# Performance work log

Hardware: AMD Instinct MI355X
Metric: run time of the kernel (lower is better)

The kernel has to match this reference:

```python
import jax, jax.numpy as jnp
import numpy as np

PI = 3.1415  # the module hard-codes 3.1415, not math.pi


def setup_inputs() -> dict:
    nt, ns, nh, ng = 1000, 1024, 64, 32
    key = jax.random.key(0)
    kP, kE, kT1, kT2, kxc, kW, kb = jax.random.split(key, 7)
    # physically plausible forcings: P, E >= 0; T2 > T1 always
    P = jax.random.uniform(kP, (nt, ns)) * 10.0
    E = jax.random.uniform(kE, (nt, ns)) * 5.0
    T1 = jax.random.normal(kT1, (nt, ns)) * 10.0
    T2 = T1 + jax.random.uniform(kT2, (nt, ns)) * 10.0 + 0.1
    x = jnp.stack([P, E, T1, T2], axis=-1)  # [nt, ns, 4]
    xc = jax.random.normal(kxc, (ns, ng))
    std = 1.0 / np.sqrt(nh)  # reset_parameters: uniform(-std, std)
    W3 = jax.random.uniform(kW, (nh * 4, ng), minval=-std, maxval=std)
    b3 = jax.random.uniform(kb, (nh * 4,), minval=-std, maxval=std)
    return {"x": x, "xc": xc, "W3": W3, "b3": b3}


def reference(x, xc, W3, b3):
    nh = W3.shape[0] // 4
    P, E, T1, T2 = x[..., 0], x[..., 1], x[..., 2], x[..., 3]  # each [nt, ns]
    Ta = (T1 + T2) * 0.5
    melted = T1 >= 0.0
    frozen = T2 <= 0.0
    masked = melted | frozen
    # NaN-safe arccos: out-of-range args occur exactly where masked overrides apply
    arg = jnp.where(masked, 0.0, jnp.clip((T1 + T2) / (T2 - T1), -1.0, 1.0))
    rP = 1.0 - jnp.arccos(arg) / PI
    rP = jnp.where(melted, 1.0, jnp.where(frozen, 0.0, rP))
    Ps = (1.0 - rP) * P  # snow fraction
    Pl = rP * P          # liquid fraction
    # static gates (fc3 on catchment attributes); dropout is identity in eval
    w = xc @ W3.T + b3  # [ns, 4*nh]
    gm = jnp.exp(w[:, :nh]) + 1.0
    ge = jax.nn.sigmoid(w[:, nh:2 * nh])
    go = jax.nn.sigmoid(w[:, 2 * nh:3 * nh])
    ga = jax.nn.softmax(w[:, 3 * nh:], axis=1)

    ns = P.shape[1]
    S0 = jnp.zeros((ns, nh), dtype=x.dtype)
    H0 = jnp.zeros((ns, nh), dtype=x.dtype)

    def step(carry, inp):
        S0, H0 = carry
        Ps_k, Pl_k, E_k, Ta_k = inp  # each [ns]
        Sm = jnp.minimum(S0, jax.nn.relu(Ta_k[:, None] * gm))  # snowmelt
        S = S0 + Ps_k[:, None]
        H = jax.nn.relu(H0 + Sm + Pl_k[:, None] - E_k[:, None] * ge)
        Q = H * go
        Y = jnp.sum(Q * ga, axis=1)  # [ns]
        return (S - Sm, H - Q), Y

    _, Yout = jax.lax.scan(step, (S0, H0), (Ps, Pl, E, Ta))
    return Yout  # [nt, ns]
```

## Files before the change

kernel.cpp:

```cpp
#include <hip/hip_runtime.h>
#include <math.h>

#define NH 64
#define NG 32
#define YROW 68

__global__ __launch_bounds__(128) void waternet_kernel(
    const float* __restrict__ x,
    const float* __restrict__ xc,
    const float* __restrict__ W3,
    const float* __restrict__ b3,
    float* __restrict__ out,
    int nt, int ns)
{
    const int b    = blockIdx.x;
    const int s    = (b & 7) * (ns >> 3) + (b >> 3);
    const int tid  = threadIdx.x;
    const int lane = tid & 63;
    const bool crit = (tid < 64);

    __shared__ float ytile[2][NH * YROW];
    __shared__ float scal[2][NH * 4];
    __shared__ float gqbuf[NH];

    float wq[4];
    #pragma unroll
    for (int q = 0; q < 4; ++q) {
        const float4* row = reinterpret_cast<const float4*>(W3 + (size_t)(q * NH + lane) * NG);
        const float4* xr  = reinterpret_cast<const float4*>(xc + (size_t)s * NG);
        float a = 0.f;
        #pragma unroll
        for (int g = 0; g < NG / 4; ++g) {
            const float4 w  = row[g];
            const float4 xv = xr[g];
            a = fmaf(w.x, xv.x, a); a = fmaf(w.y, xv.y, a);
            a = fmaf(w.z, xv.z, a); a = fmaf(w.w, xv.w, a);
        }
        wq[q] = a + b3[q * NH + lane];
    }
    const float gm = expf(wq[0]) + 1.0f;
    const float ge = 1.0f / (1.0f + expf(-wq[1]));
    const float go = 1.0f / (1.0f + expf(-wq[2]));
    float mx = wq[3];
    #pragma unroll
    for (int o = 32; o; o >>= 1) mx = fmaxf(mx, __shfl_xor(mx, o, 64));
    const float ex = expf(wq[3] - mx);
    float smx = ex;
    #pragma unroll
    for (int o = 32; o; o >>= 1) smx += __shfl_xor(smx, o, 64);
    const float ga = ex / smx;
    const float gq = go * ga;
    const float gk = 1.0f - go;

    if (!crit) gqbuf[lane] = gq;

    const int nchunk = (nt + NH - 1) / NH;

    #define PHASE_A(f, dst) { \
        const float P = (f).x, E = (f).y, T1 = (f).z, T2 = (f).w; \
        const float Ta  = 0.5f * (T1 + T2); \
        const float arg = fminf(1.f, fmaxf(-1.f, (T1 + T2) / (T2 - T1))); \
        const float aa  = fabsf(arg); \
        float p = fmaf(aa, -0.0012624911f, 0.0066700901f); \
        p = fmaf(aa, p, -0.0170881256f); p = fmaf(aa, p, 0.0308918810f); \
        p = fmaf(aa, p, -0.0501743046f); p = fmaf(aa, p, 0.0889789874f); \
        p = fmaf(aa, p, -0.2145988016f); p = fmaf(aa, p, 1.5707963050f); \
        const float rr0 = sqrtf(1.f - aa) * p; \
        const float ac  = (arg >= 0.f) ? rr0 : (3.14159265358979f - rr0); \
        const float rr  = 1.f - ac * (1.0f / 3.1415f);           \
        const float rP  = (T1 >= 0.f) ? 1.f : ((T2 <= 0.f) ? 0.f : rr); \
        float4 st; st.x = fmaxf(Ta, 0.f); st.y = (1.f - rP) * P; \
        st.z = rP * P;  st.w = E; \
        *reinterpret_cast<float4*>(&(dst)[lane * 4]) = st; \
    }

    #define LOAD8(dst, sp, j0) { \
        _Pragma("unroll") \
        for (int k = 0; k < 8; ++k) \
            dst[k] = *reinterpret_cast<const float4*>(&(sp)[((j0) + k) * 4]); \
    }

    #define STEP(sc) { \
        const float M  = (sc).x * gm; \
        const float Sm = fminf(S, M); \
        S = (S - Sm) + (sc).y; \
        const float t2 = Sm + (sc).z; \
        const float t3 = fmaf(-(sc).w, ge, t2); \
        Hc = fmaxf(fmaf(gk, Hc, t3), 0.f); \
    }

    if (!crit) {
        const int tp = min(lane, nt - 1);
        const float4 f = *reinterpret_cast<const float4*>(x + ((size_t)tp * ns + s) * 4);
        PHASE_A(f, scal[0])
    }
    __syncthreads();

    float S = 0.f, Hc = 0.f;

    #pragma unroll 1
    for (int c = 0; c < nchunk; ++c) {
        const int cnt = min(NH, nt - c * NH);
        if (crit) {
            const float* sp = scal[c & 1];
            float*       yb = &ytile[c & 1][lane * YROW];
            if (cnt == NH) {
                float4 sc[8], scn[8];
                LOAD8(sc, sp, 0)
                #pragma unroll
                for (int bb = 0; bb < 8; ++bb) {
                    if (bb < 7) LOAD8(scn, sp, (bb + 1) * 8)
                    float yv[8];
                    #pragma unroll
                    for (int k = 0; k < 8; ++k) { STEP(sc[k]) yv[k] = Hc; }
                    *reinterpret_cast<float4*>(yb + bb * 8)     = make_float4(yv[0], yv[1], yv[2], yv[3]);
                    *reinterpret_cast<float4*>(yb + bb * 8 + 4) = make_float4(yv[4], yv[5], yv[6], yv[7]);
                    if (bb < 7) {
                        #pragma unroll
                        for (int k = 0; k < 8; ++k) sc[k] = scn[k];
                    }
                }
            } else {
                const int nb = cnt / 8;
                for (int bb = 0; bb < nb; ++bb) {
                    float4 sc[8];
                    LOAD8(sc, sp, bb * 8)
                    float yv[8];
                    #pragma unroll
                    for (int k = 0; k < 8; ++k) { STEP(sc[k]) yv[k] = Hc; }
                    *reinterpret_cast<float4*>(yb + bb * 8)     = make_float4(yv[0], yv[1], yv[2], yv[3]);
                    *reinterpret_cast<float4*>(yb + bb * 8 + 4) = make_float4(yv[4], yv[5], yv[6], yv[7]);
                }
                for (int j = nb * 8; j < cnt; ++j) {
                    const float4 sc = *reinterpret_cast<const float4*>(&sp[j * 4]);
                    STEP(sc)
                    yb[j] = Hc;
                }
            }
        } else {
            const int tp = min((c + 1) * NH + lane, nt - 1);
            const float4 f = *reinterpret_cast<const float4*>(x + ((size_t)tp * ns + s) * 4);
            if (c >= 1) {
                const float* yr = ytile[(c - 1) & 1];
                float z0 = 0.f, z1 = 0.f, z2 = 0.f, z3 = 0.f;
                #pragma unroll
                for (int h = 0; h < NH; h += 4) {
                    z0 = fmaf(gqbuf[h + 0], yr[(h + 0) * YROW + lane], z0);
                    z1 = fmaf(gqbuf[h + 1], yr[(h + 1) * YROW + lane], z1);
                    z2 = fmaf(gqbuf[h + 2], yr[(h + 2) * YROW + lane], z2);
                    z3 = fmaf(gqbuf[h + 3], yr[(h + 3) * YROW + lane], z3);
                }
                out[(size_t)((c - 1) * NH + lane) * ns + s] = (z0 + z1) + (z2 + z3);
            }
            PHASE_A(f, scal[(c + 1) & 1])
        }
        __syncthreads();
    }

    if (!crit) {
        const int c   = nchunk - 1;
        const int cnt = nt - c * NH;
        const float* yr = ytile[c & 1];
        float z0 = 0.f, z1 = 0.f, z2 = 0.f, z3 = 0.f;
        #pragma unroll
        for (int h = 0; h < NH; h += 4) {
            z0 = fmaf(gqbuf[h + 0], yr[(h + 0) * YROW + lane], z0);
            z1 = fmaf(gqbuf[h + 1], yr[(h + 1) * YROW + lane], z1);
            z2 = fmaf(gqbuf[h + 2], yr[(h + 2) * YROW + lane], z2);
            z3 = fmaf(gqbuf[h + 3], yr[(h + 3) * YROW + lane], z3);
        }
        if (lane < cnt)
            out[(size_t)(c * NH + lane) * ns + s] = (z0 + z1) + (z2 + z3);
    }
    #undef PHASE_A
    #undef LOAD8
    #undef STEP
}

extern "C" void kernel_launch(void* const* d_in, const int* in_sizes, int n_in,
                              void* d_out, int out_size, void* d_ws, size_t ws_size,
                              hipStream_t stream) {
    const float* x  = (const float*)d_in[0];
    const float* xc = (const float*)d_in[1];
    const float* W3 = (const float*)d_in[2];
    const float* b3 = (const float*)d_in[3];
    float* out = (float*)d_out;

    const int nh = in_sizes[3] / 4;
    const int ng = in_sizes[2] / (4 * nh);
    const int ns = in_sizes[1] / ng;
    const int nt = in_sizes[0] / (ns * 4);

    waternet_kernel<<<dim3(ns), dim3(128), 0, stream>>>(x, xc, W3, b3, out, nt, ns);
}
```

Before: 101.7 us.

## Move forcing preprocessing into critical wave and broadcast via readlane

The critical wavefront now loads and preprocesses its own chunk of forcings in registers, then broadcasts per-timestep values to all lanes with readlane instead of reading float4 records from shared memory. The reduction wave likewise broadcasts the gq weights with readlane instead of reading an LDS buffer. This removes the scal/gqbuf shared arrays and the LDS loads from the serial recurrence. In exchange the critical wave takes on the arccos preprocessing and global load latency, which were previously overlapped on the helper wave, and readlane into SGPRs may serialize differently.

```diff
diff --git a/kernel.cpp b/kernel.cpp
--- a/kernel.cpp
+++ b/kernel.cpp
@@ -4,6 +4,10 @@
 #define NH 64
 #define NG 32
 #define YROW 68
+
+__device__ __forceinline__ float bcast(float v, int l) {
+    return __int_as_float(__builtin_amdgcn_readlane(__float_as_int(v), l));
+}
 
 __global__ __launch_bounds__(128) void waternet_kernel(
     const float* __restrict__ x,
@@ -20,8 +24,6 @@
     const bool crit = (tid < 64);
 
     __shared__ float ytile[2][NH * YROW];
-    __shared__ float scal[2][NH * 4];
-    __shared__ float gqbuf[NH];
 
     float wq[4];
     #pragma unroll
@@ -52,12 +54,11 @@
     const float gq = go * ga;
     const float gk = 1.0f - go;
 
-    if (!crit) gqbuf[lane] = gq;
-
     const int nchunk = (nt + NH - 1) / NH;
 
-    #define PHASE_A(f, dst) { \
-        const float P = (f).x, E = (f).y, T1 = (f).z, T2 = (f).w; \
+    #define PHASE_A_REG(f) { \
+        const float P = (f).x; Ev = (f).y; \
+        const float T1 = (f).z, T2 = (f).w; \
         const float Ta  = 0.5f * (T1 + T2); \
         const float arg = fminf(1.f, fmaxf(-1.f, (T1 + T2) / (T2 - T1))); \
         const float aa  = fabsf(arg); \
@@ -65,96 +66,99 @@
         p = fmaf(aa, p, -0.0170881256f); p = fmaf(aa, p, 0.0308918810f); \
         p = fmaf(aa, p, -0.0501743046f); p = fmaf(aa, p, 0.0889789874f); \
         p = fmaf(aa, p, -0.2145988016f); p = fmaf(aa, p, 1.5707963050f); \
-        const float rr0 = sqrtf(1.f - aa) * p; \
+        const float rr0 = sqrtf(1.f - aa) * p;                   \
         const float ac  = (arg >= 0.f) ? rr0 : (3.14159265358979f - rr0); \
         const float rr  = 1.f - ac * (1.0f / 3.1415f);           \
         const float rP  = (T1 >= 0.f) ? 1.f : ((T2 <= 0.f) ? 0.f : rr); \
-        float4 st; st.x = fmaxf(Ta, 0.f); st.y = (1.f - rP) * P; \
-        st.z = rP * P;  st.w = E; \
-        *reinterpret_cast<float4*>(&(dst)[lane * 4]) = st; \
+        Tr = fmaxf(Ta, 0.f); Ps = (1.f - rP) * P; Pl = rP * P; \
     }
 
-    #define LOAD8(dst, sp, j0) { \
-        _Pragma("unroll") \
-        for (int k = 0; k < 8; ++k) \
-            dst[k] = *reinterpret_cast<const float4*>(&(sp)[((j0) + k) * 4]); \
+    #define STEP(sT, sP, sL, sE) { \
+        const float M  = (sT) * gm; \
+        const float Sm = fminf(S, M); \
+        S = (S - Sm) + (sP); \
+        const float qv = fmaf(-(sE), ge, Sm); \
+        Hc = fmaxf(fmaf(gk, Hc, qv + (sL)), 0.f); \
     }
 
-    #define STEP(sc) { \
-        const float M  = (sc).x * gm; \
-        const float Sm = fminf(S, M); \
-        S = (S - Sm) + (sc).y; \
-        const float t2 = Sm + (sc).z; \
-        const float t3 = fmaf(-(sc).w, ge, t2); \
-        Hc = fmaxf(fmaf(gk, Hc, t3), 0.f); \
-    }
+    if (crit) {
+        float S = 0.f, Hc = 0.f;
+        float Tr, Ps, Pl, Ev;
 
-    if (!crit) {
-        const int tp = min(lane, nt - 1);
-        const float4 f = *reinterpret_cast<const float4*>(x + ((size_t)tp * ns + s) * 4);
-        PHASE_A(f, scal[0])
-    }
-    __syncthreads();
+        int tp = min(lane, nt - 1);
+        float4 f = *reinterpret_cast<const float4*>(x + ((size_t)tp * ns + s) * 4);
 
-    float S = 0.f, Hc = 0.f;
+        #pragma unroll 1
+        for (int c = 0; c < nchunk; ++c) {
+            const int cnt = min(NH, nt - c * NH);
+            PHASE_A_REG(f)
 
-    #pragma unroll 1
-    for (int c = 0; c < nchunk; ++c) {
-        const int cnt = min(NH, nt - c * NH);
-        if (crit) {
-            const float* sp = scal[c & 1];
-            float*       yb = &ytile[c & 1][lane * YROW];
+            tp = min((c + 1) * NH + lane, nt - 1);
+            const float4 fn = *reinterpret_cast<const float4*>(x + ((size_t)tp * ns + s) * 4);
+
+            float* yb = &ytile[c & 1][lane * YROW];
+
             if (cnt == NH) {
-                float4 sc[8], scn[8];
-                LOAD8(sc, sp, 0)
                 #pragma unroll
                 for (int bb = 0; bb < 8; ++bb) {
-                    if (bb < 7) LOAD8(scn, sp, (bb + 1) * 8)
+                    float sT[8], sP[8], sL[8], sE[8];
+                    #pragma unroll
+                    for (int k = 0; k < 8; ++k) {
+                        sT[k] = bcast(Tr, bb * 8 + k);
+                        sP[k] = bcast(Ps, bb * 8 + k);
+                        sL[k] = bcast(Pl, bb * 8 + k);
+                        sE[k] = bcast(Ev, bb * 8 + k);
+                    }
                     float yv[8];
                     #pragma unroll
-                    for (int k = 0; k < 8; ++k) { STEP(sc[k]) yv[k] = Hc; }
+                    for (int k = 0; k < 8; ++k) { STEP(sT[k], sP[k], sL[k], sE[k]) yv[k] = Hc; }
                     *reinterpret_cast<float4*>(yb + bb * 8)     = make_float4(yv[0], yv[1], yv[2], yv[3]);
                     *reinterpret_cast<float4*>(yb + bb * 8 + 4) = make_float4(yv[4], yv[5], yv[6], yv[7]);
-                    if (bb < 7) {
-                        #pragma unroll
-                        for (int k = 0; k < 8; ++k) sc[k] = scn[k];
-                    }
                 }
             } else {
                 const int nb = cnt / 8;
                 for (int bb = 0; bb < nb; ++bb) {
-                    float4 sc[8];
-                    LOAD8(sc, sp, bb * 8)
+                    float sT[8], sP[8], sL[8], sE[8];
+                    #pragma unroll
+                    for (int k = 0; k < 8; ++k) {
+                        sT[k] = bcast(Tr, bb * 8 + k);
+                        sP[k] = bcast(Ps, bb * 8 + k);
+                        sL[k] = bcast(Pl, bb * 8 + k);
+                        sE[k] = bcast(Ev, bb * 8 + k);
+                    }
                     float yv[8];
                     #pragma unroll
-                    for (int k = 0; k < 8; ++k) { STEP(sc[k]) yv[k] = Hc; }
+                    for (int k = 0; k < 8; ++k) { STEP(sT[k], sP[k], sL[k], sE[k]) yv[k] = Hc; }
                     *reinterpret_cast<float4*>(yb + bb * 8)     = make_float4(yv[0], yv[1], yv[2], yv[3]);
                     *reinterpret_cast<float4*>(yb + bb * 8 + 4) = make_float4(yv[4], yv[5], yv[6], yv[7]);
                 }
                 for (int j = nb * 8; j < cnt; ++j) {
-                    const float4 sc = *reinterpret_cast<const float4*>(&sp[j * 4]);
-                    STEP(sc)
+                    const float sT = bcast(Tr, j), sP = bcast(Ps, j);
+                    const float sL = bcast(Pl, j), sE = bcast(Ev, j);
+                    STEP(sT, sP, sL, sE)
                     yb[j] = Hc;
                 }
             }
-        } else {
-            const int tp = min((c + 1) * NH + lane, nt - 1);
-            const float4 f = *reinterpret_cast<const float4*>(x + ((size_t)tp * ns + s) * 4);
+            f = fn;
+            __syncthreads();
+        }
+    } else {
+        #pragma unroll 1
+        for (int c = 0; c < nchunk; ++c) {
             if (c >= 1) {
                 const float* yr = ytile[(c - 1) & 1];
                 float z0 = 0.f, z1 = 0.f, z2 = 0.f, z3 = 0.f;
                 #pragma unroll
                 for (int h = 0; h < NH; h += 4) {
-                    z0 = fmaf(gqbuf[h + 0], yr[(h + 0) * YROW + lane], z0);
-                    z1 = fmaf(gqbuf[h + 1], yr[(h + 1) * YROW + lane], z1);
-                    z2 = fmaf(gqbuf[h + 2], yr[(h + 2) * YROW + lane], z2);
-                    z3 = fmaf(gqbuf[h + 3], yr[(h + 3) * YROW + lane], z3);
+                    z0 = fmaf(bcast(gq, h + 0), yr[(h + 0) * YROW + lane], z0);
+                    z1 = fmaf(bcast(gq, h + 1), yr[(h + 1) * YROW + lane], z1);
+                    z2 = fmaf(bcast(gq, h + 2), yr[(h + 2) * YROW + lane], z2);
+                    z3 = fmaf(bcast(gq, h + 3), yr[(h + 3) * YROW + lane], z3);
                 }
                 out[(size_t)((c - 1) * NH + lane) * ns + s] = (z0 + z1) + (z2 + z3);
             }
-            PHASE_A(f, scal[(c + 1) & 1])
+            __syncthreads();
         }
-        __syncthreads();
     }
 
     if (!crit) {
@@ -164,16 +168,15 @@
         float z0 = 0.f, z1 = 0.f, z2 = 0.f, z3 = 0.f;
         #pragma unroll
         for (int h = 0; h < NH; h += 4) {
-            z0 = fmaf(gqbuf[h + 0], yr[(h + 0) * YROW + lane], z0);
-            z1 = fmaf(gqbuf[h + 1], yr[(h + 1) * YROW + lane], z1);
-            z2 = fmaf(gqbuf[h + 2], yr[(h + 2) * YROW + lane], z2);
-            z3 = fmaf(gqbuf[h + 3], yr[(h + 3) * YROW + lane], z3);
+            z0 = fmaf(bcast(gq, h + 0), yr[(h + 0) * YROW + lane], z0);
+            z1 = fmaf(bcast(gq, h + 1), yr[(h + 1) * YROW + lane], z1);
+            z2 = fmaf(bcast(gq, h + 2), yr[(h + 2) * YROW + lane], z2);
+            z3 = fmaf(bcast(gq, h + 3), yr[(h + 3) * YROW + lane], z3);
         }
         if (lane < cnt)
             out[(size_t)(c * NH + lane) * ns + s] = (z0 + z1) + (z2 + z3);
     }
-    #undef PHASE_A
-    #undef LOAD8
+    #undef PHASE_A_REG
     #undef STEP
 }
 
```

Result: slower. 110.1 us (+8.3%).

## Split forcing preprocessing into separate kernel and stream scan inputs from global

Applied to the files above, without the earlier changes.

Moves the per-timestep snow/rain partition (arccos polynomial) into its own fully parallel kernel that writes a preprocessed buffer to workspace. The recurrent scan wave then reads float4 inputs straight from global memory with register prefetch, instead of waiting on a helper wave to fill shared memory. The helper wave now only does the gated output reduction, and gq is broadcast with readlane instead of going through a shared buffer. This adds a second launch plus a full write and reread of a 16 MB intermediate, and the scan's strided global loads may stall the serial chain if the prefetch does not hide their latency. A fallback kernel keeps the old path when the workspace is too small.

```diff
diff --git a/kernel.cpp b/kernel.cpp
--- a/kernel.cpp
+++ b/kernel.cpp
@@ -5,8 +5,38 @@
 #define NG 32
 #define YROW 68
 
+__device__ __forceinline__ float bcast(float v, int l) {
+    return __int_as_float(__builtin_amdgcn_readlane(__float_as_int(v), l));
+}
+
+__global__ __launch_bounds__(256) void phasea_kernel(
+    const float* __restrict__ x, float* __restrict__ scr, int n )
+{
+    const int i = blockIdx.x * 256 + threadIdx.x;
+    if (i >= n) return;
+    const float4 f = reinterpret_cast<const float4*>(x)[i];
+    const float P = f.x, E = f.y, T1 = f.z, T2 = f.w;
+    const float Ta  = 0.5f * (T1 + T2);
+    const float arg = fminf(1.f, fmaxf(-1.f, (T1 + T2) / (T2 - T1)));
+    const float aa  = fabsf(arg);
+    float p = fmaf(aa, -0.0012624911f, 0.0066700901f);
+    p = fmaf(aa, p, -0.0170881256f); p = fmaf(aa, p, 0.0308918810f);
+    p = fmaf(aa, p, -0.0501743046f); p = fmaf(aa, p, 0.0889789874f);
+    p = fmaf(aa, p, -0.2145988016f); p = fmaf(aa, p, 1.5707963050f);
+    const float rr0 = sqrtf(1.f - aa) * p;
+    const float ac  = (arg >= 0.f) ? rr0 : (3.14159265358979f - rr0);
+    const float rr  = 1.f - ac * (1.0f / 3.1415f);
+    const float rP  = (T1 >= 0.f) ? 1.f : ((T2 <= 0.f) ? 0.f : rr);
+    float4 st;
+    st.x = fmaxf(Ta, 0.f);
+    st.y = (1.f - rP) * P;
+    st.z = rP * P;
+    st.w = E;
+    reinterpret_cast<float4*>(scr)[i] = st;
+}
+
 __global__ __launch_bounds__(128) void waternet_kernel(
-    const float* __restrict__ x,
+    const float* __restrict__ scr,
     const float* __restrict__ xc,
     const float* __restrict__ W3,
     const float* __restrict__ b3,
@@ -20,8 +50,6 @@
     const bool crit = (tid < 64);
 
     __shared__ float ytile[2][NH * YROW];
-    __shared__ float scal[2][NH * 4];
-    __shared__ float gqbuf[NH];
 
     float wq[4];
     #pragma unroll
@@ -52,11 +80,136 @@
     const float gq = go * ga;
     const float gk = 1.0f - go;
 
+    const int nchunk = (nt + NH - 1) / NH;
+
+    #define STEP(sc) { \
+        const float M  = (sc).x * gm; \
+        const float Sm = fminf(S, M); \
+        S = (S - Sm) + (sc).y; \
+        const float qv = fmaf(-(sc).w, ge, Sm); \
+        Hc = fmaxf(fmaf(gk, Hc, qv + (sc).z), 0.f); \
+    }
+    #define LOADB(dst, g) { \
+        _Pragma("unroll") \
+        for (int k = 0; k < 8; ++k) \
+            dst[k] = sp[(size_t)((g) + k) * ns];    \
+    }
+
+    if (crit) {
+        const float4* sp = reinterpret_cast<const float4*>(scr) + s;
+        float S = 0.f, Hc = 0.f;
+        float4 sc[8], scn[8];
+        const int nb_all = nt / 8;
+        LOADB(sc, 0)
+
+        #pragma unroll 1
+        for (int c = 0; c < nchunk; ++c) {
+            const int cnt = min(NH, nt - c * NH);
+            float* yb = &ytile[c & 1][lane * YROW];
+            const int nb = cnt / 8;
+
+            #pragma unroll 1
+            for (int bb = 0; bb < nb; ++bb) {
+                const int g = c * NH + bb * 8;
+                if ((g >> 3) + 1 < nb_all) LOADB(scn, g + 8)
+
+                float yv[8];
+                #pragma unroll
+                for (int k = 0; k < 8; ++k) { STEP(sc[k]) yv[k] = Hc; }
+                *reinterpret_cast<float4*>(yb + bb * 8)     = make_float4(yv[0], yv[1], yv[2], yv[3]);
+                *reinterpret_cast<float4*>(yb + bb * 8 + 4) = make_float4(yv[4], yv[5], yv[6], yv[7]);
+
+                #pragma unroll
+                for (int k = 0; k < 8; ++k) sc[k] = scn[k];
+            }
+            for (int j = nb * 8; j < cnt; ++j) {
+                const float4 scr1 = sp[(size_t)(c * NH + j) * ns];
+                STEP(scr1)
+                yb[j] = Hc;
+            }
+            __syncthreads();
+        }
+    } else {
+        #pragma unroll 1
+        for (int c = 0; c < nchunk; ++c) {
+            if (c >= 1) {
+                const float* yr = ytile[(c - 1) & 1];
+                float z0 = 0.f, z1 = 0.f, z2 = 0.f, z3 = 0.f;
+                #pragma unroll
+                for (int h = 0; h < NH; h += 4) {
+                    z0 = fmaf(bcast(gq, h + 0), yr[(h + 0) * YROW + lane], z0);
+                    z1 = fmaf(bcast(gq, h + 1), yr[(h + 1) * YROW + lane], z1);
+                    z2 = fmaf(bcast(gq, h + 2), yr[(h + 2) * YROW + lane], z2);
+                    z3 = fmaf(bcast(gq, h + 3), yr[(h + 3) * YROW + lane], z3);
+                }
+                out[(size_t)((c - 1) * NH + lane) * ns + s] = (z0 + z1) + (z2 + z3);
+            }
+            __syncthreads();
+        }
+        const int c   = nchunk - 1;
+        const int cnt = nt - c * NH;
+        const float* yr = ytile[c & 1];
+        float z0 = 0.f, z1 = 0.f, z2 = 0.f, z3 = 0.f;
+        #pragma unroll
+        for (int h = 0; h < NH; h += 4) {
+            z0 = fmaf(bcast(gq, h + 0), yr[(h + 0) * YROW + lane], z0);
+            z1 = fmaf(bcast(gq, h + 1), yr[(h + 1) * YROW + lane], z1);
+            z2 = fmaf(bcast(gq, h + 2), yr[(h + 2) * YROW + lane], z2);
+            z3 = fmaf(bcast(gq, h + 3), yr[(h + 3) * YROW + lane], z3);
+        }
+        if (lane < cnt)
+            out[(size_t)(c * NH + lane) * ns + s] = (z0 + z1) + (z2 + z3);
+    }
+    #undef STEP
+    #undef LOADB
+}
+
+__global__ __launch_bounds__(128) void waternet_fallback(
+    const float* __restrict__ x, const float* __restrict__ xc,
+    const float* __restrict__ W3, const float* __restrict__ b3,
+    float* __restrict__ out, int nt, int ns)
+{
+    const int b    = blockIdx.x;
+    const int s    = (b & 7) * (ns >> 3) + (b >> 3);
+    const int tid  = threadIdx.x;
+    const int lane = tid & 63;
+    const bool crit = (tid < 64);
+
+    __shared__ float ytile[2][NH * YROW];
+    __shared__ float scal[2][NH * 4];
+    __shared__ float gqbuf[NH];
+
+    float wq[4];
+    #pragma unroll
+    for (int q = 0; q < 4; ++q) {
+        const float4* row = reinterpret_cast<const float4*>(W3 + (size_t)(q * NH + lane) * NG);
+        const float4* xr  = reinterpret_cast<const float4*>(xc + (size_t)s * NG);
+        float a = 0.f;
+        #pragma unroll
+        for (int g = 0; g < NG / 4; ++g) {
+            const float4 w = row[g]; const float4 xv = xr[g];
+            a = fmaf(w.x, xv.x, a); a = fmaf(w.y, xv.y, a);
+            a = fmaf(w.z, xv.z, a); a = fmaf(w.w, xv.w, a);
+        }
+        wq[q] = a + b3[q * NH + lane];
+    }
+    const float gm = expf(wq[0]) + 1.0f;
+    const float ge = 1.0f / (1.0f + expf(-wq[1]));
+    const float go = 1.0f / (1.0f + expf(-wq[2]));
+    float mx = wq[3];
+    #pragma unroll
+    for (int o = 32; o; o >>= 1) mx = fmaxf(mx, __shfl_xor(mx, o, 64));
+    const float ex = expf(wq[3] - mx);
+    float smx = ex;
+    #pragma unroll
+    for (int o = 32; o; o >>= 1) smx += __shfl_xor(smx, o, 64);
+    const float gq = go * (ex / smx);
+    const float gk = 1.0f - go;
     if (!crit) gqbuf[lane] = gq;
 
     const int nchunk = (nt + NH - 1) / NH;
 
-    #define PHASE_A(f, dst) { \
+    #define FPA(f, dst) { \
         const float P = (f).x, E = (f).y, T1 = (f).z, T2 = (f).w; \
         const float Ta  = 0.5f * (T1 + T2); \
         const float arg = fminf(1.f, fmaxf(-1.f, (T1 + T2) / (T2 - T1))); \
@@ -67,75 +220,49 @@
         p = fmaf(aa, p, -0.2145988016f); p = fmaf(aa, p, 1.5707963050f); \
         const float rr0 = sqrtf(1.f - aa) * p; \
         const float ac  = (arg >= 0.f) ? rr0 : (3.14159265358979f - rr0); \
-        const float rr  = 1.f - ac * (1.0f / 3.1415f);           \
+        const float rr  = 1.f - ac * (1.0f / 3.1415f); \
         const float rP  = (T1 >= 0.f) ? 1.f : ((T2 <= 0.f) ? 0.f : rr); \
         float4 st; st.x = fmaxf(Ta, 0.f); st.y = (1.f - rP) * P; \
         st.z = rP * P;  st.w = E; \
         *reinterpret_cast<float4*>(&(dst)[lane * 4]) = st; \
     }
-
-    #define LOAD8(dst, sp, j0) { \
-        _Pragma("unroll") \
-        for (int k = 0; k < 8; ++k) \
-            dst[k] = *reinterpret_cast<const float4*>(&(sp)[((j0) + k) * 4]); \
-    }
-
-    #define STEP(sc) { \
+    #define FSTEP(sc) { \
         const float M  = (sc).x * gm; \
         const float Sm = fminf(S, M); \
         S = (S - Sm) + (sc).y; \
-        const float t2 = Sm + (sc).z; \
-        const float t3 = fmaf(-(sc).w, ge, t2); \
-        Hc = fmaxf(fmaf(gk, Hc, t3), 0.f); \
+        const float qv = fmaf(-(sc).w, ge, Sm); \
+        Hc = fmaxf(fmaf(gk, Hc, qv + (sc).z), 0.f); \
     }
 
     if (!crit) {
         const int tp = min(lane, nt - 1);
         const float4 f = *reinterpret_cast<const float4*>(x + ((size_t)tp * ns + s) * 4);
-        PHASE_A(f, scal[0])
+        FPA(f, scal[0])
     }
     __syncthreads();
 
     float S = 0.f, Hc = 0.f;
-
     #pragma unroll 1
     for (int c = 0; c < nchunk; ++c) {
         const int cnt = min(NH, nt - c * NH);
         if (crit) {
             const float* sp = scal[c & 1];
             float*       yb = &ytile[c & 1][lane * YROW];
-            if (cnt == NH) {
-                float4 sc[8], scn[8];
-                LOAD8(sc, sp, 0)
-                #pragma unroll
-                for (int bb = 0; bb < 8; ++bb) {
-                    if (bb < 7) LOAD8(scn, sp, (bb + 1) * 8)
-                    float yv[8];
-                    #pragma unroll
-                    for (int k = 0; k < 8; ++k) { STEP(sc[k]) yv[k] = Hc; }
-                    *reinterpret_cast<float4*>(yb + bb * 8)     = make_float4(yv[0], yv[1], yv[2], yv[3]);
-                    *reinterpret_cast<float4*>(yb + bb * 8 + 4) = make_float4(yv[4], yv[5], yv[6], yv[7]);
-                    if (bb < 7) {
-                        #pragma unroll
-                        for (int k = 0; k < 8; ++k) sc[k] = scn[k];
-                    }
-                }
-            } else {
-                const int nb = cnt / 8;
-                for (int bb = 0; bb < nb; ++bb) {
-                    float4 sc[8];
-                    LOAD8(sc, sp, bb * 8)
-                    float yv[8];
-                    #pragma unroll
-                    for (int k = 0; k < 8; ++k) { STEP(sc[k]) yv[k] = Hc; }
-                    *reinterpret_cast<float4*>(yb + bb * 8)     = make_float4(yv[0], yv[1], yv[2], yv[3]);
-                    *reinterpret_cast<float4*>(yb + bb * 8 + 4) = make_float4(yv[4], yv[5], yv[6], yv[7]);
-                }
-                for (int j = nb * 8; j < cnt; ++j) {
-                    const float4 sc = *reinterpret_cast<const float4*>(&sp[j * 4]);
-                    STEP(sc)
-                    yb[j] = Hc;
-                }
+            const int nb = cnt / 8;
+            for (int bb = 0; bb < nb; ++bb) {
+                float4 sc[8];
+                #pragma unroll
+                for (int k = 0; k < 8; ++k)
+                    sc[k] = *reinterpret_cast<const float4*>(&sp[(bb * 8 + k) * 4]);
+                float yv[8];
+                #pragma unroll
+                for (int k = 0; k < 8; ++k) { FSTEP(sc[k]) yv[k] = Hc; }
+                *reinterpret_cast<float4*>(yb + bb * 8)     = make_float4(yv[0], yv[1], yv[2], yv[3]);
+                *reinterpret_cast<float4*>(yb + bb * 8 + 4) = make_float4(yv[4], yv[5], yv[6], yv[7]);
+            }
+            for (int j = nb * 8; j < cnt; ++j) {
+                const float4 sc = *reinterpret_cast<const float4*>(&sp[j * 4]);
+                FSTEP(sc) yb[j] = Hc;
             }
         } else {
             const int tp = min((c + 1) * NH + lane, nt - 1);
@@ -152,14 +279,12 @@
                 }
                 out[(size_t)((c - 1) * NH + lane) * ns + s] = (z0 + z1) + (z2 + z3);
             }
-            PHASE_A(f, scal[(c + 1) & 1])
+            FPA(f, scal[(c + 1) & 1])
         }
         __syncthreads();
     }
-
     if (!crit) {
-        const int c   = nchunk - 1;
-        const int cnt = nt - c * NH;
+        const int c = nchunk - 1, cnt = nt - c * NH;
         const float* yr = ytile[c & 1];
         float z0 = 0.f, z1 = 0.f, z2 = 0.f, z3 = 0.f;
         #pragma unroll
@@ -172,9 +297,8 @@
         if (lane < cnt)
             out[(size_t)(c * NH + lane) * ns + s] = (z0 + z1) + (z2 + z3);
     }
-    #undef PHASE_A
-    #undef LOAD8
-    #undef STEP
+    #undef FPA
+    #undef FSTEP
 }
 
 extern "C" void kernel_launch(void* const* d_in, const int* in_sizes, int n_in,
@@ -191,5 +315,13 @@
     const int ns = in_sizes[1] / ng;
     const int nt = in_sizes[0] / (ns * 4);
 
-    waternet_kernel<<<dim3(ns), dim3(128), 0, stream>>>(x, xc, W3, b3, out, nt, ns);
-}
+    const size_t need = (size_t)nt * ns * 4 * sizeof(float);
+    if (ws_size >= need) {
+        float* scr = (float*)d_ws;
+        const int n = nt * ns;
+        phasea_kernel<<<dim3((n + 255) / 256), dim3(256), 0, stream>>>(x, scr, n);
+        waternet_kernel<<<dim3(ns), dim3(128), 0, stream>>>(scr, xc, W3, b3, out, nt, ns);
+    } else {
+        waternet_fallback<<<dim3(ns), dim3(128), 0, stream>>>(x, xc, W3, b3, out, nt, ns);
+    }
+}
```

Result: slower. 145.2 us (+42.8%).
